# Kernel optimization log

Measured on AMD Instinct MI355X. Metric: run time of the kernel, lower is better.

Reference implementation:

```python
import jax, jax.numpy as jnp
import numpy as np

N = 100000
E = 1600000
IN_DIM = 128
OUT_DIM = 128
NEG_SLOPE = 0.01  # F.leaky_relu default


def setup_inputs() -> dict:
    key = jax.random.key(0)
    k1, k2, k3, k4, k5, k6 = jax.random.split(key, 6)
    feat = jax.random.normal(k1, (N, IN_DIM), dtype=jnp.float32)
    biclique_mask = jax.random.uniform(k2, (IN_DIM,), dtype=jnp.float32)
    W = jax.random.normal(k3, (OUT_DIM, IN_DIM), dtype=jnp.float32) * 0.05
    attn = jax.random.normal(k4, (OUT_DIM,), dtype=jnp.float32) * 0.1
    src = jax.random.randint(k5, (E,), 0, N, dtype=jnp.int32)
    dst = jax.random.randint(k6, (E,), 0, N, dtype=jnp.int32)
    return {"feat": feat, "biclique_mask": biclique_mask, "W": W,
            "attn": attn, "src": src, "dst": dst}


def reference(feat, biclique_mask, W, attn, src, dst):
    # h = Linear(feat * mask), no bias
    h = (feat * biclique_mask[None, :]) @ W.T            # [N, out_dim]
    # edge score depends only on src node -> compute per-node then gather
    s = jax.nn.leaky_relu(h @ attn, negative_slope=NEG_SLOPE)  # [N]
    score = s[src]                                        # [E]
    # edge softmax grouped by destination node
    seg_max = jax.ops.segment_max(score, dst, num_segments=N)  # [N]
    seg_max = jnp.where(jnp.isfinite(seg_max), seg_max, 0.0)   # empty segs
    ex = jnp.exp(score - seg_max[dst])                     # [E]
    denom = jax.ops.segment_sum(ex, dst, num_segments=N)   # [N]
    a = ex / denom[dst]                                    # [E]
    # weighted aggregation: sum_{e: dst(e)=v} h[src(e)] * a[e]
    m = h[src] * a[:, None]                                # [E, out_dim]
    h_new = jax.ops.segment_sum(m, dst, num_segments=N)    # [N, out_dim]
    return jax.nn.relu(h_new)
```

## Files before the change

kernel.cpp:

```cpp
#include <hip/hip_runtime.h>
#include <math.h>

#define NN 100000
#define EE 1600000
#define DIM 128

#define BK 256
#define NBK2 392
#define NCH 256
#define EPB 6250
#define SCN (NBK2 * NCH)
#define NSB 98

typedef _Float16 half8 __attribute__((ext_vector_type(8)));
typedef float f32x4 __attribute__((ext_vector_type(4)));

__global__ __launch_bounds__(256) void k_wt(const float* __restrict__ W,
                                            const float* __restrict__ mask,
                                            _Float16* __restrict__ Bt) {
    int o = blockIdx.x * 256 + threadIdx.x;
    if (o < DIM * DIM) Bt[o] = (_Float16)(W[o] * mask[o & 127]);
}

__global__ __launch_bounds__(256) void k_gemm(const float* __restrict__ feat,
                                              const _Float16* __restrict__ Bt,
                                              const float* __restrict__ attn,
                                              _Float16* __restrict__ hh,
                                              float* __restrict__ s) {
    const int lane = threadIdx.x & 63;
    const int wv   = threadIdx.x >> 6;
    const int l15  = lane & 15;
    const int quad = lane >> 4;
    const int row0 = blockIdx.x * 64 + wv * 16;

    f32x4 acc[8];
#pragma unroll
    for (int nt = 0; nt < 8; ++nt) acc[nt] = (f32x4){0.f, 0.f, 0.f, 0.f};

    const int arow = row0 + l15;
    const bool okA = arow < NN;
    const float* ap = feat + (size_t)(okA ? arow : 0) * DIM + quad * 8;

#pragma unroll
    for (int kc = 0; kc < 4; ++kc) {
        half8 a;
        float4 f0 = ((const float4*)(ap + kc * 32))[0];
        float4 f1 = ((const float4*)(ap + kc * 32))[1];
        if (!okA) { f0 = make_float4(0, 0, 0, 0); f1 = make_float4(0, 0, 0, 0); }
        a[0] = (_Float16)f0.x; a[1] = (_Float16)f0.y;
        a[2] = (_Float16)f0.z; a[3] = (_Float16)f0.w;
        a[4] = (_Float16)f1.x; a[5] = (_Float16)f1.y;
        a[6] = (_Float16)f1.z; a[7] = (_Float16)f1.w;
#pragma unroll
        for (int nt = 0; nt < 8; ++nt) {
            half8 b = *(const half8*)(Bt + (size_t)(nt * 16 + l15) * DIM + kc * 32 + quad * 8);
            acc[nt] = __builtin_amdgcn_mfma_f32_16x16x32_f16(a, b, acc[nt], 0, 0, 0);
        }
    }

    float avv[8];
#pragma unroll
    for (int nt = 0; nt < 8; ++nt) avv[nt] = attn[nt * 16 + l15];

#pragma unroll
    for (int r = 0; r < 4; ++r) {
        int row = row0 + quad * 4 + r;
        float p = 0.f;
#pragma unroll
        for (int nt = 0; nt < 8; ++nt) p += acc[nt][r] * avv[nt];
        p += __shfl_xor(p, 1, 64);
        p += __shfl_xor(p, 2, 64);
        p += __shfl_xor(p, 4, 64);
        p += __shfl_xor(p, 8, 64);
        if (l15 == 0 && row < NN) {
            float lr = (p > 0.f) ? p : 0.01f * p;
            s[row] = __expf(lr);
        }
    }

#pragma unroll
    for (int nt = 0; nt < 8; ++nt) {
#pragma unroll
        for (int r = 0; r < 4; ++r) {
            int row = row0 + quad * 4 + r;
            if (row < NN)
                hh[(size_t)row * DIM + nt * 16 + l15] = (_Float16)acc[nt][r];
        }
    }
}

__global__ __launch_bounds__(1024) void k_bhist(const int* __restrict__ dst,
                                                int* __restrict__ gHist) {
    __shared__ int hist[NBK2];
    const int t = threadIdx.x, b = blockIdx.x;
    for (int i = t; i < NBK2; i += 1024) hist[i] = 0;
    __syncthreads();
    const int e0 = b * EPB;
    int e1 = e0 + EPB; if (e1 > EE) e1 = EE;
    for (int e = e0 + t; e < e1; e += 1024)
        atomicAdd(&hist[dst[e] >> 8], 1);
    __syncthreads();
    for (int i = t; i < NBK2; i += 1024)
        gHist[i * NCH + b] = hist[i];
}

__global__ __launch_bounds__(256) void k_scan_a(const int* __restrict__ deg,
                                                int* __restrict__ excl,
                                                int* __restrict__ bsum) {
    __shared__ int wsum[4];
    __shared__ int woff[4];
    const int t = threadIdx.x, b = blockIdx.x;
    const int base = b * 1024 + t * 4;
    int v0 = deg[base + 0];
    int v1 = deg[base + 1];
    int v2 = deg[base + 2];
    int v3 = deg[base + 3];
    int tsum = v0 + v1 + v2 + v3;

    const int lane = t & 63, w = t >> 6;
    int incl = tsum;
#pragma unroll
    for (int d = 1; d < 64; d <<= 1) {
        int n = __shfl_up(incl, d, 64);
        if (lane >= d) incl += n;
    }
    if (lane == 63) wsum[w] = incl;
    __syncthreads();
    if (t == 0) {
        int run = 0;
#pragma unroll
        for (int i = 0; i < 4; ++i) { woff[i] = run; run += wsum[i]; }
        bsum[b] = run;
    }
    __syncthreads();
    int texcl = incl - tsum + woff[w];
    excl[base + 0] = texcl;
    excl[base + 1] = texcl + v0;
    excl[base + 2] = texcl + v0 + v1;
    excl[base + 3] = texcl + v0 + v1 + v2;
}

__global__ __launch_bounds__(128) void k_scan_b(const int* __restrict__ bsum,
                                                int* __restrict__ boff) {
    __shared__ int wtop[2];
    const int t = threadIdx.x;
    const int lane = t & 63, w = t >> 6;
    int v = (t < NSB) ? bsum[t] : 0;
    int incl = v;
#pragma unroll
    for (int d = 1; d < 64; d <<= 1) {
        int n = __shfl_up(incl, d, 64);
        if (lane >= d) incl += n;
    }
    if (lane == 63) wtop[w] = incl;
    __syncthreads();
    int add = (w == 1) ? wtop[0] : 0;
    if (t < NSB) boff[t] = incl - v + add;
}

__global__ __launch_bounds__(1024) void k_bscatter(const int* __restrict__ src,
                                                   const int* __restrict__ dst,
                                                   const float* __restrict__ s,
                                                   const int* __restrict__ gOff,
                                                   const int* __restrict__ boff,
                                                   int2* __restrict__ binned) {
    __shared__ int cur[NBK2];
    const int t = threadIdx.x, b = blockIdx.x;
    for (int i = t; i < NBK2; i += 1024) {
        int idx = i * NCH + b;
        cur[i] = gOff[idx] + boff[idx >> 10];
    }
    __syncthreads();
    const int e0 = b * EPB;
    int e1 = e0 + EPB; if (e1 > EE) e1 = EE;
    for (int e = e0 + t; e < e1; e += 1024) {
        int d  = dst[e];
        int si = src[e];
        float x = s[si];
        int bk   = d >> 8;
        int dloc = d & (BK - 1);
        int pos = atomicAdd(&cur[bk], 1);
        binned[pos] = make_int2(si | (dloc << 20), __float_as_int(x));
    }
}

__global__ __launch_bounds__(1024) void k_group(const int* __restrict__ gOff,
                                                const int* __restrict__ boff,
                                                const int2* __restrict__ binned,
                                                int2* __restrict__ pack,
                                                int* __restrict__ offs) {
    __shared__ int ldeg[BK];
    __shared__ int wpart[4];
    const int bk = blockIdx.x;
    const int t  = threadIdx.x;
    const int i0 = bk * NCH;
    const int base = gOff[i0] + boff[i0 >> 10];
    int endp;
    if (bk == NBK2 - 1) endp = EE;
    else {
        int i1 = (bk + 1) * NCH;
        endp = gOff[i1] + boff[i1 >> 10];
    }

    if (t < BK) ldeg[t] = 0;
    __syncthreads();
    for (int j = base + t; j < endp; j += 1024)
        atomicAdd(&ldeg[(binned[j].x >> 20) & (BK - 1)], 1);
    __syncthreads();

    int v = 0, incl = 0;
    const int lane = t & 63;
    if (t < BK) {
        v = ldeg[t];
        incl = v;
#pragma unroll
        for (int d = 1; d < 64; d <<= 1) {
            int n = __shfl_up(incl, d, 64);
            if (lane >= d) incl += n;
        }
        if (lane == 63) wpart[t >> 6] = incl;
    }
    __syncthreads();
    if (t == 0) {
        int run = 0;
#pragma unroll
        for (int i = 0; i < 4; ++i) { int tmp = wpart[i]; wpart[i] = run; run += tmp; }
    }
    __syncthreads();
    if (t < BK) {
        int excl = incl - v + wpart[t >> 6];
        int c = base + excl;
        int n = bk * BK + t;
        if (n < NN) offs[n] = c;
        ldeg[t] = c;
    }
    if (bk == NBK2 - 1 && t == 0) offs[NN] = EE;
    __syncthreads();

    for (int j = base + t; j < endp; j += 1024) {
        int2 e = binned[j];
        int dloc = (e.x >> 20) & (BK - 1);
        int si   = e.x & 0xFFFFF;
        int pos = atomicAdd(&ldeg[dloc], 1);
        pack[pos] = make_int2(si, e.y);
    }
}

__global__ __launch_bounds__(256) void k_agg(const _Float16* __restrict__ hh,
                                             const int* __restrict__ offs,
                                             const int2* __restrict__ pack,
                                             float* __restrict__ out) {
    const int lane = threadIdx.x & 63;
    const int g    = lane >> 4;
    const int li   = lane & 15;
    const int wid  = __builtin_amdgcn_readfirstlane(blockIdx.x * 4 + (threadIdx.x >> 6));
    if (wid >= NN) return;
    const int beg = __builtin_amdgcn_readfirstlane(offs[wid]);
    const int end = __builtin_amdgcn_readfirstlane(offs[wid + 1]);
    const int deg = end - beg;

    const half8* h8 = (const half8*)hh;
    float acc[8];
#pragma unroll
    for (int k = 0; k < 8; ++k) acc[k] = 0.f;
    float lsum = 0.f;

    for (int base = 0; base < deg; base += 64) {
        const int nrem = deg - base;
        const int idx  = base + lane;
        const int cl   = (idx < deg) ? idx : (deg - 1);
        const int2 e   = pack[beg + cl];
        const float w  = (idx < deg) ? __int_as_float(e.y) : 0.f;
        lsum += w;
        const int cmax = (nrem < 64) ? nrem : 64;
        for (int c0 = 0; c0 < cmax; c0 += 16) {
#pragma unroll
            for (int s = 0; s < 4; ++s) {
                const int ei = c0 + s * 4 + g;
                const int   si = __shfl(e.x, ei, 64);
                const float wg = __shfl(w,   ei, 64);
                half8 v = h8[((unsigned)si << 4) + li];
#pragma unroll
                for (int k = 0; k < 8; ++k)
                    acc[k] = fmaf((float)v[k], wg, acc[k]);
            }
        }
    }

#pragma unroll
    for (int k = 0; k < 8; ++k) {
        acc[k] += __shfl_xor(acc[k], 16, 64);
        acc[k] += __shfl_xor(acc[k], 32, 64);
    }
    lsum += __shfl_xor(lsum, 1, 64);
    lsum += __shfl_xor(lsum, 2, 64);
    lsum += __shfl_xor(lsum, 4, 64);
    lsum += __shfl_xor(lsum, 8, 64);
    lsum += __shfl_xor(lsum, 16, 64);
    lsum += __shfl_xor(lsum, 32, 64);

    const float inv = (lsum > 0.f) ? (1.0f / lsum) : 0.f;

    if (g == 0) {
        float4 o0, o1;
        o0.x = fmaxf(acc[0] * inv, 0.f);
        o0.y = fmaxf(acc[1] * inv, 0.f);
        o0.z = fmaxf(acc[2] * inv, 0.f);
        o0.w = fmaxf(acc[3] * inv, 0.f);
        o1.x = fmaxf(acc[4] * inv, 0.f);
        o1.y = fmaxf(acc[5] * inv, 0.f);
        o1.z = fmaxf(acc[6] * inv, 0.f);
        o1.w = fmaxf(acc[7] * inv, 0.f);
        float4* op = (float4*)(out + (size_t)wid * DIM + li * 8);
        op[0] = o0;
        op[1] = o1;
    }
}

extern "C" void kernel_launch(void* const* d_in, const int* in_sizes, int n_in,
                              void* d_out, int out_size, void* d_ws, size_t ws_size,
                              hipStream_t stream) {
    const float* feat = (const float*)d_in[0];
    const float* mask = (const float*)d_in[1];
    const float* W    = (const float*)d_in[2];
    const float* attn = (const float*)d_in[3];
    const int*   src  = (const int*)d_in[4];
    const int*   dst  = (const int*)d_in[5];
    float* out = (float*)d_out;

    char* ws = (char*)d_ws;
    size_t off = 0;
    auto alloc = [&](size_t bytes) -> void* {
        void* p = ws + off;
        off = (off + bytes + 511) & ~(size_t)511;
        return p;
    };
    _Float16* hh  = (_Float16*)alloc((size_t)NN * DIM * 2);
    float*  sv    = (float*)alloc((size_t)NN * 4);
    _Float16* Bt  = (_Float16*)alloc((size_t)DIM * DIM * 2);
    int*    gOff  = (int*)alloc((size_t)SCN * 4);
    int*    offs  = (int*)alloc((size_t)(NN + 1) * 4);
    int*    bsum  = (int*)alloc((size_t)NSB * 4);
    int*    boff  = (int*)alloc((size_t)NSB * 4);
    int2*   binned= (int2*)alloc((size_t)EE * 8);
    int2*   pack  = (int2*)alloc((size_t)EE * 8);

    k_wt<<<(DIM * DIM + 255) / 256, 256, 0, stream>>>(W, mask, Bt);
    k_gemm<<<(NN + 63) / 64, 256, 0, stream>>>(feat, Bt, attn, hh, sv);
    k_bhist<<<NCH, 1024, 0, stream>>>(dst, gOff);
    k_scan_a<<<NSB, 256, 0, stream>>>(gOff, gOff, bsum);
    k_scan_b<<<1, 128, 0, stream>>>(bsum, boff);
    k_bscatter<<<NCH, 1024, 0, stream>>>(src, dst, sv, gOff, boff, binned);
    k_group<<<NBK2, 1024, 0, stream>>>(gOff, boff, binned, pack, offs);
    k_agg<<<(NN + 3) / 4, 256, 0, stream>>>(hh, offs, pack, out);
}
```

Before: 245.5 us.

## Pack edge records into 32 bits with fp16 weight and defer score gather

```diff
diff --git a/kernel.cpp b/kernel.cpp
--- a/kernel.cpp
+++ b/kernel.cpp
@@ -12,6 +12,8 @@
 #define SCN (NBK2 * NCH)
 #define NSB 98
 
+#define SRC_MASK 0x1FFFFu
+
 typedef _Float16 half8 __attribute__((ext_vector_type(8)));
 typedef float f32x4 __attribute__((ext_vector_type(4)));
 
@@ -26,7 +28,7 @@
                                               const _Float16* __restrict__ Bt,
                                               const float* __restrict__ attn,
                                               _Float16* __restrict__ hh,
-                                              float* __restrict__ s) {
+                                              _Float16* __restrict__ sv16) {
     const int lane = threadIdx.x & 63;
     const int wv   = threadIdx.x >> 6;
     const int l15  = lane & 15;
@@ -74,7 +76,7 @@
         p += __shfl_xor(p, 8, 64);
         if (l15 == 0 && row < NN) {
             float lr = (p > 0.f) ? p : 0.01f * p;
-            s[row] = __expf(lr);
+            sv16[row] = (_Float16)__expf(lr);
         }
     }
 
@@ -160,10 +162,9 @@
 
 __global__ __launch_bounds__(1024) void k_bscatter(const int* __restrict__ src,
                                                    const int* __restrict__ dst,
-                                                   const float* __restrict__ s,
                                                    const int* __restrict__ gOff,
                                                    const int* __restrict__ boff,
-                                                   int2* __restrict__ binned) {
+                                                   unsigned* __restrict__ binned) {
     __shared__ int cur[NBK2];
     const int t = threadIdx.x, b = blockIdx.x;
     for (int i = t; i < NBK2; i += 1024) {
@@ -176,18 +177,18 @@
     for (int e = e0 + t; e < e1; e += 1024) {
         int d  = dst[e];
         int si = src[e];
-        float x = s[si];
         int bk   = d >> 8;
         int dloc = d & (BK - 1);
         int pos = atomicAdd(&cur[bk], 1);
-        binned[pos] = make_int2(si | (dloc << 20), __float_as_int(x));
+        binned[pos] = (unsigned)si | ((unsigned)dloc << 17);
     }
 }
 
 __global__ __launch_bounds__(1024) void k_group(const int* __restrict__ gOff,
                                                 const int* __restrict__ boff,
-                                                const int2* __restrict__ binned,
-                                                int2* __restrict__ pack,
+                                                const unsigned* __restrict__ binned,
+                                                const _Float16* __restrict__ sv16,
+                                                unsigned* __restrict__ pack,
                                                 int* __restrict__ offs) {
     __shared__ int ldeg[BK];
     __shared__ int wpart[4];
@@ -205,7 +206,7 @@
     if (t < BK) ldeg[t] = 0;
     __syncthreads();
     for (int j = base + t; j < endp; j += 1024)
-        atomicAdd(&ldeg[(binned[j].x >> 20) & (BK - 1)], 1);
+        atomicAdd(&ldeg[(binned[j] >> 17) & (BK - 1)], 1);
     __syncthreads();
 
     int v = 0, incl = 0;
@@ -238,17 +239,19 @@
     __syncthreads();
 
     for (int j = base + t; j < endp; j += 1024) {
-        int2 e = binned[j];
-        int dloc = (e.x >> 20) & (BK - 1);
-        int si   = e.x & 0xFFFFF;
+        unsigned e = binned[j];
+        int dloc = (e >> 17) & (BK - 1);
+        int si   = e & SRC_MASK;
+        unsigned short wb =
+            __builtin_bit_cast(unsigned short, sv16[si]);
         int pos = atomicAdd(&ldeg[dloc], 1);
-        pack[pos] = make_int2(si, e.y);
+        pack[pos] = (unsigned)si | ((unsigned)wb << 17);
     }
 }
 
 __global__ __launch_bounds__(256) void k_agg(const _Float16* __restrict__ hh,
                                              const int* __restrict__ offs,
-                                             const int2* __restrict__ pack,
+                                             const unsigned* __restrict__ pack,
                                              float* __restrict__ out) {
     const int lane = threadIdx.x & 63;
     const int g    = lane >> 4;
@@ -269,16 +272,20 @@
         const int nrem = deg - base;
         const int idx  = base + lane;
         const int cl   = (idx < deg) ? idx : (deg - 1);
-        const int2 e   = pack[beg + cl];
-        const float w  = (idx < deg) ? __int_as_float(e.y) : 0.f;
-        lsum += w;
+        const unsigned eraw = pack[beg + cl];
+        const unsigned enc = (idx < deg) ? eraw : (eraw & SRC_MASK);
+        lsum += (float)__builtin_bit_cast(_Float16,
+                                          (unsigned short)(enc >> 17));
         const int cmax = (nrem < 64) ? nrem : 64;
         for (int c0 = 0; c0 < cmax; c0 += 16) {
 #pragma unroll
             for (int s = 0; s < 4; ++s) {
                 const int ei = c0 + s * 4 + g;
-                const int   si = __shfl(e.x, ei, 64);
-                const float wg = __shfl(w,   ei, 64);
+                const unsigned eb =
+                    (unsigned)__shfl((int)enc, ei, 64);
+                const int   si = eb & SRC_MASK;
+                const float wg = (float)__builtin_bit_cast(
+                    _Float16, (unsigned short)(eb >> 17));
                 half8 v = h8[((unsigned)si << 4) + li];
 #pragma unroll
                 for (int k = 0; k < 8; ++k)
@@ -335,22 +342,22 @@
         off = (off + bytes + 511) & ~(size_t)511;
         return p;
     };
-    _Float16* hh  = (_Float16*)alloc((size_t)NN * DIM * 2);
-    float*  sv    = (float*)alloc((size_t)NN * 4);
-    _Float16* Bt  = (_Float16*)alloc((size_t)DIM * DIM * 2);
-    int*    gOff  = (int*)alloc((size_t)SCN * 4);
-    int*    offs  = (int*)alloc((size_t)(NN + 1) * 4);
-    int*    bsum  = (int*)alloc((size_t)NSB * 4);
-    int*    boff  = (int*)alloc((size_t)NSB * 4);
-    int2*   binned= (int2*)alloc((size_t)EE * 8);
-    int2*   pack  = (int2*)alloc((size_t)EE * 8);
+    _Float16* hh   = (_Float16*)alloc((size_t)NN * DIM * 2);
+    _Float16* sv16 = (_Float16*)alloc((size_t)NN * 2);
+    _Float16* Bt   = (_Float16*)alloc((size_t)DIM * DIM * 2);
+    int*     gOff  = (int*)alloc((size_t)SCN * 4);
+    int*     offs  = (int*)alloc((size_t)(NN + 1) * 4);
+    int*     bsum  = (int*)alloc((size_t)NSB * 4);
+    int*     boff  = (int*)alloc((size_t)NSB * 4);
+    unsigned* binned = (unsigned*)alloc((size_t)EE * 4);
+    unsigned* pack   = (unsigned*)alloc((size_t)EE * 4);
 
     k_wt<<<(DIM * DIM + 255) / 256, 256, 0, stream>>>(W, mask, Bt);
-    k_gemm<<<(NN + 63) / 64, 256, 0, stream>>>(feat, Bt, attn, hh, sv);
+    k_gemm<<<(NN + 63) / 64, 256, 0, stream>>>(feat, Bt, attn, hh, sv16);
     k_bhist<<<NCH, 1024, 0, stream>>>(dst, gOff);
     k_scan_a<<<NSB, 256, 0, stream>>>(gOff, gOff, bsum);
     k_scan_b<<<1, 128, 0, stream>>>(bsum, boff);
-    k_bscatter<<<NCH, 1024, 0, stream>>>(src, dst, sv, gOff, boff, binned);
-    k_group<<<NBK2, 1024, 0, stream>>>(gOff, boff, binned, pack, offs);
+    k_bscatter<<<NCH, 1024, 0, stream>>>(src, dst, gOff, boff, binned);
+    k_group<<<NBK2, 1024, 0, stream>>>(gOff, boff, binned, sv16, pack, offs);
     k_agg<<<(NN + 3) / 4, 256, 0, stream>>>(hh, offs, pack, out);
 }
```

Measured after the change: 237.6 us. 3.2% less time.
